# Optimization experiments

Measured on AMD Instinct MI355X. Metric: run time of the kernel, lower is better.

The kernel has to match this reference:

```python
import jax, jax.numpy as jnp
import numpy as np

N_CLASSES = 1000
FEAT_DIM = 256
N = 65536


def setup_inputs() -> dict:
    key = jax.random.key(0)
    k1, k2, k3 = jax.random.split(key, 3)
    gt = jax.random.randint(k1, (N, N_CLASSES), 0, 2, dtype=jnp.int32)
    features = jax.random.normal(k2, (N, FEAT_DIM), dtype=jnp.float32)
    centers = jax.random.normal(k3, (N_CLASSES, FEAT_DIM), dtype=jnp.float32)
    return {"gt": gt, "features": features, "centers": centers}


def reference(gt, features, centers):
    # loss = (1/N) * sum_c sum_{i : gt[i,c] > 0} ||features[i] - centers[c]||^2
    # Vectorized via ||f||^2 + ||c||^2 - 2 f.c  (replaces the per-class python loop)
    mask = (gt > 0).astype(features.dtype)                      # [N, C]
    f_sq = jnp.sum(features * features, axis=1)                 # [N]
    c_sq = jnp.sum(centers * centers, axis=1)                   # [C]
    cross = features @ centers.T                                # [N, C]
    dist = f_sq[:, None] + c_sq[None, :] - 2.0 * cross          # [N, C]
    num_instances = features.shape[0]
    return jnp.sum(mask * dist) / num_instances
```

## Files before the change

kernel.cpp:

```cpp
#include <hip/hip_runtime.h>
#include <stdint.h>

#define N_ROWS 65536
#define N_CLS  1000
#define KPAD   1024
#define FEAT   256
#define MT     64
#define BK     64
#define NIT    (KPAD/BK)

typedef _Float16 f16x8 __attribute__((ext_vector_type(8)));
typedef _Float16 f16x2 __attribute__((ext_vector_type(2)));
typedef float    f32x4 __attribute__((ext_vector_type(4)));

__device__ __forceinline__ f16x2 as_f16x2(uint32_t u) {
    union { uint32_t u; f16x2 h; } c; c.u = u; return c.h;
}

__global__ __launch_bounds__(256) void prep_kernel(const float* __restrict__ centers,
                                                   ushort* __restrict__ centersT,
                                                   ushort* __restrict__ csqh,
                                                   float* __restrict__ out) {
    const int c = blockIdx.x;
    const int n = threadIdx.x;
    float v = 0.f;
    if (c < N_CLS) v = centers[(size_t)c * FEAT + n];
    union { _Float16 h; ushort s; } cv; cv.h = (_Float16)v;
    centersT[(size_t)n * KPAD + c] = cv.s;
    float sq = v * v;
    #pragma unroll
    for (int off = 32; off > 0; off >>= 1) sq += __shfl_down(sq, off);
    __shared__ float red[4];
    if ((threadIdx.x & 63) == 0) red[threadIdx.x >> 6] = sq;
    __syncthreads();
    if (threadIdx.x == 0) {
        union { _Float16 h; ushort s; } cs;
        cs.h = (_Float16)(red[0] + red[1] + red[2] + red[3]);
        csqh[c] = cs.s;
        if (c == 0) out[0] = 0.f;
    }
}

__global__ __launch_bounds__(256, 4) void main_kernel(const int* __restrict__ gt,
                                                      const float* __restrict__ features,
                                                      const ushort* __restrict__ centersT,
                                                      const ushort* __restrict__ csqh,
                                                      float* __restrict__ out) {
    __shared__ uint4 As4[MT * 8];
    __shared__ uint4 Bs4[FEAT * 8];

    const int tid  = threadIdx.x;
    const int m0   = blockIdx.x * MT;
    const int r    = tid >> 2;
    const int kc2  = tid & 3;
    const int lane = tid & 63;
    const int w    = tid >> 6;
    const int ml   = lane & 15;
    const int quad = lane >> 4;
    const int mls  = ml & 7;

    f32x4 acc[4][4];
    #pragma unroll
    for (int i = 0; i < 4; i++)
        #pragma unroll
        for (int j = 0; j < 4; j++)
            #pragma unroll
            for (int k = 0; k < 4; k++) acc[i][j][k] = 0.f;

    uint32_t rcp = 0;
    float    t2  = 0.f;
    const int*   gtrow = gt + (size_t)(m0 + r) * N_CLS;
    const uint4* ctv   = (const uint4*)centersT;

    for (int it = 0; it < NIT; ++it) {
        const int k0 = it * BK;
        const int kb = k0 + kc2 * 16;
        __syncthreads();

        int v[16];
        if (kb + 16 <= N_CLS) {
            const int4* p = (const int4*)(gtrow + kb);
            int4 a0 = p[0], a1 = p[1], a2 = p[2], a3 = p[3];
            v[0]=a0.x; v[1]=a0.y; v[2]=a0.z; v[3]=a0.w;
            v[4]=a1.x; v[5]=a1.y; v[6]=a1.z; v[7]=a1.w;
            v[8]=a2.x; v[9]=a2.y; v[10]=a2.z; v[11]=a2.w;
            v[12]=a3.x; v[13]=a3.y; v[14]=a3.z; v[15]=a3.w;
        } else {
            #pragma unroll
            for (int j = 0; j < 16; j++) {
                int k = kb + j;
                v[j] = (k < N_CLS) ? gtrow[k] : 0;
            }
        }
        uint4 cq0 = *(const uint4*)(csqh + kb);
        uint4 cq1 = *(const uint4*)(csqh + kb + 8);
        uint32_t cp[8] = {cq0.x, cq0.y, cq0.z, cq0.w, cq1.x, cq1.y, cq1.z, cq1.w};

        uint32_t u[8];
        #pragma unroll
        for (int j = 0; j < 8; j++) {
            uint32_t t = (uint32_t)v[2*j] + ((uint32_t)v[2*j+1] << 16);
            rcp += t;
            u[j] = t * 0x3C00u;
            t2 = __builtin_amdgcn_fdot2(as_f16x2(u[j]), as_f16x2(cp[j]), t2, false);
        }

        {
            uint4* dst = &As4[r * 8];
            dst[(2*kc2)     ^ (r & 7)] = make_uint4(u[0], u[1], u[2], u[3]);
            dst[(2*kc2 + 1) ^ (r & 7)] = make_uint4(u[4], u[5], u[6], u[7]);
        }

        #pragma unroll
        for (int j = 0; j < 8; j++) {
            int g  = j * 256 + tid;
            int n  = g >> 3;
            int kl = g & 7;
            Bs4[n * 8 + (kl ^ (n & 7))] = ctv[n * 128 + (k0 >> 3) + kl];
        }

        __syncthreads();

        #pragma unroll
        for (int ks = 0; ks < 2; ++ks) {
            const int lc = ks * 4 + quad;
            f16x8 af[4], bfr[4];
            #pragma unroll
            for (int mt = 0; mt < 4; mt++)
                af[mt] = ((const f16x8*)As4)[(mt * 16 + ml) * 8 + (lc ^ mls)];
            #pragma unroll
            for (int nt = 0; nt < 4; nt++) {
                const int col = w * 64 + nt * 16 + ml;
                bfr[nt] = ((const f16x8*)Bs4)[col * 8 + (lc ^ mls)];
            }
            #pragma unroll
            for (int mt = 0; mt < 4; mt++)
                #pragma unroll
                for (int nt = 0; nt < 4; nt++)
                    acc[mt][nt] = __builtin_amdgcn_mfma_f32_16x16x32_f16(
                        af[mt], bfr[nt], acc[mt][nt], 0, 0, 0);
        }
    }

    __syncthreads();
    float* S = (float*)As4;
    S[tid] = (float)((rcp & 0xFFFFu) + (rcp >> 16));
    __syncthreads();
    if (tid < MT)
        S[256 + tid] = S[tid*4] + S[tid*4+1] + S[tid*4+2] + S[tid*4+3];
    __syncthreads();

    float part = t2;
    #pragma unroll
    for (int mt = 0; mt < 4; mt++) {
        #pragma unroll
        for (int nt = 0; nt < 4; nt++) {
            const int n = w * 64 + nt * 16 + ml;
            #pragma unroll
            for (int reg = 0; reg < 4; reg++) {
                const int ri = mt * 16 + quad * 4 + reg;
                const float f = features[(size_t)(m0 + ri) * FEAT + n];
                const float T = acc[mt][nt][reg];
                part += f * (S[256 + ri] * f - 2.f * T);
            }
        }
    }
    #pragma unroll
    for (int off = 32; off > 0; off >>= 1) part += __shfl_down(part, off);
    if (lane == 0) S[320 + w] = part;
    __syncthreads();
    if (tid == 0)
        atomicAdd(out, (S[320] + S[321] + S[322] + S[323]) * (1.f / (float)N_ROWS));
}

extern "C" void kernel_launch(void* const* d_in, const int* in_sizes, int n_in,
                              void* d_out, int out_size, void* d_ws, size_t ws_size,
                              hipStream_t stream) {
    const int*   gt       = (const int*)d_in[0];
    const float* features = (const float*)d_in[1];
    const float* centers  = (const float*)d_in[2];
    float*       out      = (float*)d_out;

    ushort* centersT = (ushort*)d_ws;
    ushort* csqh     = (ushort*)((char*)d_ws + (size_t)FEAT * KPAD * 2);

    prep_kernel<<<KPAD, 256, 0, stream>>>(centers, centersT, csqh, out);
    main_kernel<<<N_ROWS / MT, 256, 0, stream>>>(gt, features, centersT, csqh, out);
}
```

Before: 434.3 us.

## Give each wave its own 16-row tile and stream centers from global into registers

Each wave now handles its own 16 rows across all 256 features. The centers operand is loaded straight from global or L2 into registers with double buffering, instead of being staged through shared memory behind block-wide barriers. The next gt tile is prefetched into registers while the current MFMAs run, and the row-count reduction is done with wave shuffles. This removes the per-iteration __syncthreads and the shared-memory B staging. In exchange it uses more registers (occupancy hint lowered to 2) and does redundant global reads of centers per wave.

```diff
diff --git a/kernel.cpp b/kernel.cpp
--- a/kernel.cpp
+++ b/kernel.cpp
@@ -41,136 +41,149 @@
     }
 }
 
-__global__ __launch_bounds__(256, 4) void main_kernel(const int* __restrict__ gt,
+__global__ __launch_bounds__(256, 2) void main_kernel(const int* __restrict__ gt,
                                                       const float* __restrict__ features,
                                                       const ushort* __restrict__ centersT,
                                                       const ushort* __restrict__ csqh,
                                                       float* __restrict__ out) {
-    __shared__ uint4 As4[MT * 8];
-    __shared__ uint4 Bs4[FEAT * 8];
+    __shared__ uint4 As4[4][16 * 8];
+    __shared__ float red[4];
 
     const int tid  = threadIdx.x;
-    const int m0   = blockIdx.x * MT;
-    const int r    = tid >> 2;
-    const int kc2  = tid & 3;
     const int lane = tid & 63;
     const int w    = tid >> 6;
+    const int r    = lane >> 2;
+    const int kc   = lane & 3;
     const int ml   = lane & 15;
     const int quad = lane >> 4;
     const int mls  = ml & 7;
-
-    f32x4 acc[4][4];
-    #pragma unroll
-    for (int i = 0; i < 4; i++)
-        #pragma unroll
-        for (int j = 0; j < 4; j++)
-            #pragma unroll
-            for (int k = 0; k < 4; k++) acc[i][j][k] = 0.f;
+    const int mw   = blockIdx.x * MT + w * 16;
+
+    const int*    gtrow = gt + (size_t)(mw + r) * N_CLS;
+    const ushort* cb    = centersT + (size_t)ml * KPAD + quad * 8;
+    uint4*        AsW   = As4[w];
+
+    f32x4 acc[16];
+    #pragma unroll
+    for (int i = 0; i < 16; i++)
+        #pragma unroll
+        for (int k = 0; k < 4; k++) acc[i][k] = 0.f;
 
     uint32_t rcp = 0;
     float    t2  = 0.f;
-    const int*   gtrow = gt + (size_t)(m0 + r) * N_CLS;
-    const uint4* ctv   = (const uint4*)centersT;
+
+    int4 a0, a1, a2, a3;
+    {
+        const int4* p = (const int4*)(gtrow + kc * 16);
+        a0 = p[0]; a1 = p[1]; a2 = p[2]; a3 = p[3];
+    }
+
+    f16x8 b0[8], b1[8];
+    #pragma unroll
+    for (int nt = 0; nt < 8; nt++)
+        b0[nt] = *(const f16x8*)(cb + (size_t)(nt * 16) * KPAD);
 
     for (int it = 0; it < NIT; ++it) {
         const int k0 = it * BK;
-        const int kb = k0 + kc2 * 16;
-        __syncthreads();
-
-        int v[16];
-        if (kb + 16 <= N_CLS) {
-            const int4* p = (const int4*)(gtrow + kb);
-            int4 a0 = p[0], a1 = p[1], a2 = p[2], a3 = p[3];
-            v[0]=a0.x; v[1]=a0.y; v[2]=a0.z; v[3]=a0.w;
-            v[4]=a1.x; v[5]=a1.y; v[6]=a1.z; v[7]=a1.w;
-            v[8]=a2.x; v[9]=a2.y; v[10]=a2.z; v[11]=a2.w;
-            v[12]=a3.x; v[13]=a3.y; v[14]=a3.z; v[15]=a3.w;
-        } else {
-            #pragma unroll
-            for (int j = 0; j < 16; j++) {
-                int k = kb + j;
-                v[j] = (k < N_CLS) ? gtrow[k] : 0;
-            }
-        }
+
+        #pragma unroll
+        for (int nt = 0; nt < 8; nt++)
+            b1[nt] = *(const f16x8*)(cb + (size_t)((nt + 8) * 16) * KPAD + k0);
+
+        const int kb = k0 + kc * 16;
         uint4 cq0 = *(const uint4*)(csqh + kb);
         uint4 cq1 = *(const uint4*)(csqh + kb + 8);
-        uint32_t cp[8] = {cq0.x, cq0.y, cq0.z, cq0.w, cq1.x, cq1.y, cq1.z, cq1.w};
-
+        uint32_t cs[8] = {cq0.x, cq0.y, cq0.z, cq0.w, cq1.x, cq1.y, cq1.z, cq1.w};
+
+        int v[16] = {a0.x, a0.y, a0.z, a0.w, a1.x, a1.y, a1.z, a1.w,
+                     a2.x, a2.y, a2.z, a2.w, a3.x, a3.y, a3.z, a3.w};
         uint32_t u[8];
         #pragma unroll
         for (int j = 0; j < 8; j++) {
             uint32_t t = (uint32_t)v[2*j] + ((uint32_t)v[2*j+1] << 16);
             rcp += t;
             u[j] = t * 0x3C00u;
-            t2 = __builtin_amdgcn_fdot2(as_f16x2(u[j]), as_f16x2(cp[j]), t2, false);
-        }
-
-        {
-            uint4* dst = &As4[r * 8];
-            dst[(2*kc2)     ^ (r & 7)] = make_uint4(u[0], u[1], u[2], u[3]);
-            dst[(2*kc2 + 1) ^ (r & 7)] = make_uint4(u[4], u[5], u[6], u[7]);
-        }
-
-        #pragma unroll
-        for (int j = 0; j < 8; j++) {
-            int g  = j * 256 + tid;
-            int n  = g >> 3;
-            int kl = g & 7;
-            Bs4[n * 8 + (kl ^ (n & 7))] = ctv[n * 128 + (k0 >> 3) + kl];
-        }
-
-        __syncthreads();
-
-        #pragma unroll
-        for (int ks = 0; ks < 2; ++ks) {
-            const int lc = ks * 4 + quad;
-            f16x8 af[4], bfr[4];
+            t2 = __builtin_amdgcn_fdot2(as_f16x2(u[j]), as_f16x2(cs[j]), t2, false);
+        }
+
+        AsW[r * 8 + ((2*kc)     ^ (r & 7))] = make_uint4(u[0], u[1], u[2], u[3]);
+        AsW[r * 8 + ((2*kc + 1) ^ (r & 7))] = make_uint4(u[4], u[5], u[6], u[7]);
+
+        if (it + 1 < NIT) {
+            const int kb2 = (it + 1) * BK + kc * 16;
+            if (kb2 + 16 <= N_CLS) {
+                const int4* p = (const int4*)(gtrow + kb2);
+                a0 = p[0]; a1 = p[1]; a2 = p[2]; a3 = p[3];
+            } else {
+                int t16[16];
+                #pragma unroll
+                for (int j = 0; j < 16; j++) {
+                    int k = kb2 + j;
+                    t16[j] = (k < N_CLS) ? gtrow[k] : 0;
+                }
+                a0 = make_int4(t16[0],  t16[1],  t16[2],  t16[3]);
+                a1 = make_int4(t16[4],  t16[5],  t16[6],  t16[7]);
+                a2 = make_int4(t16[8],  t16[9],  t16[10], t16[11]);
+                a3 = make_int4(t16[12], t16[13], t16[14], t16[15]);
+            }
+        }
+
+        f16x8 af0 = ((const f16x8*)AsW)[ml * 8 + ( quad      ^ mls)];
+        f16x8 af1 = ((const f16x8*)AsW)[ml * 8 + ((4 + quad) ^ mls)];
+
+        #pragma unroll
+        for (int nt = 0; nt < 8; nt++)
+            acc[nt] = __builtin_amdgcn_mfma_f32_16x16x32_f16(af0, b0[nt], acc[nt], 0, 0, 0);
+        #pragma unroll
+        for (int nt = 0; nt < 8; nt++)
+            b0[nt] = *(const f16x8*)(cb + (size_t)(nt * 16) * KPAD + k0 + 32);
+
+        #pragma unroll
+        for (int nt = 0; nt < 8; nt++)
+            acc[8+nt] = __builtin_amdgcn_mfma_f32_16x16x32_f16(af0, b1[nt], acc[8+nt], 0, 0, 0);
+        #pragma unroll
+        for (int nt = 0; nt < 8; nt++)
+            b1[nt] = *(const f16x8*)(cb + (size_t)((nt + 8) * 16) * KPAD + k0 + 32);
+
+        #pragma unroll
+        for (int nt = 0; nt < 8; nt++)
+            acc[nt] = __builtin_amdgcn_mfma_f32_16x16x32_f16(af1, b0[nt], acc[nt], 0, 0, 0);
+        if (it + 1 < NIT) {
             #pragma unroll
-            for (int mt = 0; mt < 4; mt++)
-                af[mt] = ((const f16x8*)As4)[(mt * 16 + ml) * 8 + (lc ^ mls)];
-            #pragma unroll
-            for (int nt = 0; nt < 4; nt++) {
-                const int col = w * 64 + nt * 16 + ml;
-                bfr[nt] = ((const f16x8*)Bs4)[col * 8 + (lc ^ mls)];
-            }
-            #pragma unroll
-            for (int mt = 0; mt < 4; mt++)
-                #pragma unroll
-                for (int nt = 0; nt < 4; nt++)
-                    acc[mt][nt] = __builtin_amdgcn_mfma_f32_16x16x32_f16(
-                        af[mt], bfr[nt], acc[mt][nt], 0, 0, 0);
-        }
-    }
-
-    __syncthreads();
-    float* S = (float*)As4;
-    S[tid] = (float)((rcp & 0xFFFFu) + (rcp >> 16));
-    __syncthreads();
-    if (tid < MT)
-        S[256 + tid] = S[tid*4] + S[tid*4+1] + S[tid*4+2] + S[tid*4+3];
-    __syncthreads();
+            for (int nt = 0; nt < 8; nt++)
+                b0[nt] = *(const f16x8*)(cb + (size_t)(nt * 16) * KPAD + k0 + 64);
+        }
+
+        #pragma unroll
+        for (int nt = 0; nt < 8; nt++)
+            acc[8+nt] = __builtin_amdgcn_mfma_f32_16x16x32_f16(af1, b1[nt], acc[8+nt], 0, 0, 0);
+    }
+
+    float rcf = (float)((rcp & 0xFFFFu) + (rcp >> 16));
+    rcf += __shfl_xor(rcf, 1);
+    rcf += __shfl_xor(rcf, 2);
+    float rw[4];
+    #pragma unroll
+    for (int reg = 0; reg < 4; reg++)
+        rw[reg] = __shfl(rcf, quad * 16 + reg * 4);
 
     float part = t2;
     #pragma unroll
-    for (int mt = 0; mt < 4; mt++) {
-        #pragma unroll
-        for (int nt = 0; nt < 4; nt++) {
-            const int n = w * 64 + nt * 16 + ml;
-            #pragma unroll
-            for (int reg = 0; reg < 4; reg++) {
-                const int ri = mt * 16 + quad * 4 + reg;
-                const float f = features[(size_t)(m0 + ri) * FEAT + n];
-                const float T = acc[mt][nt][reg];
-                part += f * (S[256 + ri] * f - 2.f * T);
-            }
+    for (int nt = 0; nt < 16; nt++) {
+        const int n = nt * 16 + ml;
+        #pragma unroll
+        for (int reg = 0; reg < 4; reg++) {
+            const int ri = quad * 4 + reg;
+            const float f = features[(size_t)(mw + ri) * FEAT + n];
+            part += f * (rw[reg] * f - 2.f * acc[nt][reg]);
         }
     }
     #pragma unroll
     for (int off = 32; off > 0; off >>= 1) part += __shfl_down(part, off);
-    if (lane == 0) S[320 + w] = part;
+    if (lane == 0) red[w] = part;
     __syncthreads();
     if (tid == 0)
-        atomicAdd(out, (S[320] + S[321] + S[322] + S[323]) * (1.f / (float)N_ROWS));
+        atomicAdd(out, (red[0] + red[1] + red[2] + red[3]) * (1.f / (float)N_ROWS));
 }
 
 extern "C" void kernel_launch(void* const* d_in, const int* in_sizes, int n_in,
```

Measured after the change: 582.3 us. 1.34x slower.

## Preload gt tile into LDS bitmask panel with flat coalesced loads

Applied to the files above, without the earlier changes.

Before the GEMM loop, the whole 64x1000 gt tile for the block is read with flat, fully contiguous int4 loads. Each group of 8 entries is compressed into one byte of an LDS bitmask panel, and the c_sq dot term is accumulated in fp32 at the same time. The MFMA loop then rebuilds the fp16 A fragments from those bits, and row counts come from popcounts over the panel. This removes the per-row strided gt loads and the fp16 A tile staging inside the main loop. The cost is a separate load phase that does not overlap with compute, plus bit-expansion ALU work in the inner loop.

```diff
diff --git a/kernel.cpp b/kernel.cpp
--- a/kernel.cpp
+++ b/kernel.cpp
@@ -6,20 +6,26 @@
 #define KPAD   1024
 #define FEAT   256
 #define MT     64
-#define BK     64
-#define NIT    (KPAD/BK)
+#define NIT    16
+#define PITERS 16
 
 typedef _Float16 f16x8 __attribute__((ext_vector_type(8)));
-typedef _Float16 f16x2 __attribute__((ext_vector_type(2)));
 typedef float    f32x4 __attribute__((ext_vector_type(4)));
 
-__device__ __forceinline__ f16x2 as_f16x2(uint32_t u) {
-    union { uint32_t u; f16x2 h; } c; c.u = u; return c.h;
+__device__ __forceinline__ f16x8 expand8(uint32_t b) {
+    union { uint32_t u[4]; f16x8 v; } r;
+#pragma unroll
+    for (int p = 0; p < 4; ++p) {
+        uint32_t lo = (b >> (2 * p)) & 1u;
+        uint32_t hi = (b >> (2 * p + 1)) & 1u;
+        r.u[p] = lo * 0x3C00u + hi * 0x3C000000u;
+    }
+    return r.v;
 }
 
 __global__ __launch_bounds__(256) void prep_kernel(const float* __restrict__ centers,
                                                    ushort* __restrict__ centersT,
-                                                   ushort* __restrict__ csqh,
+                                                   float* __restrict__ csqf,
                                                    float* __restrict__ out) {
     const int c = blockIdx.x;
     const int n = threadIdx.x;
@@ -28,15 +34,13 @@
     union { _Float16 h; ushort s; } cv; cv.h = (_Float16)v;
     centersT[(size_t)n * KPAD + c] = cv.s;
     float sq = v * v;
-    #pragma unroll
+#pragma unroll
     for (int off = 32; off > 0; off >>= 1) sq += __shfl_down(sq, off);
     __shared__ float red[4];
     if ((threadIdx.x & 63) == 0) red[threadIdx.x >> 6] = sq;
     __syncthreads();
     if (threadIdx.x == 0) {
-        union { _Float16 h; ushort s; } cs;
-        cs.h = (_Float16)(red[0] + red[1] + red[2] + red[3]);
-        csqh[c] = cs.s;
+        csqf[c] = red[0] + red[1] + red[2] + red[3];
         if (c == 0) out[0] = 0.f;
     }
 }
@@ -44,133 +48,139 @@
 __global__ __launch_bounds__(256, 4) void main_kernel(const int* __restrict__ gt,
                                                       const float* __restrict__ features,
                                                       const ushort* __restrict__ centersT,
-                                                      const ushort* __restrict__ csqh,
+                                                      const float* __restrict__ csqf,
                                                       float* __restrict__ out) {
-    __shared__ uint4 As4[MT * 8];
     __shared__ uint4 Bs4[FEAT * 8];
+    __shared__ uint4 panelV[512];
+    unsigned char* panel = (unsigned char*)panelV;
 
     const int tid  = threadIdx.x;
     const int m0   = blockIdx.x * MT;
-    const int r    = tid >> 2;
-    const int kc2  = tid & 3;
     const int lane = tid & 63;
     const int w    = tid >> 6;
     const int ml   = lane & 15;
     const int quad = lane >> 4;
     const int mls  = ml & 7;
 
+    panelV[tid]       = make_uint4(0, 0, 0, 0);
+    panelV[256 + tid] = make_uint4(0, 0, 0, 0);
+
     f32x4 acc[4][4];
-    #pragma unroll
+#pragma unroll
     for (int i = 0; i < 4; i++)
-        #pragma unroll
+#pragma unroll
         for (int j = 0; j < 4; j++)
-            #pragma unroll
+#pragma unroll
             for (int k = 0; k < 4; k++) acc[i][j][k] = 0.f;
 
-    uint32_t rcp = 0;
-    float    t2  = 0.f;
-    const int*   gtrow = gt + (size_t)(m0 + r) * N_CLS;
-    const uint4* ctv   = (const uint4*)centersT;
+    float t2 = 0.f;
+    const int* gtb = gt + (size_t)m0 * N_CLS;
 
-    for (int it = 0; it < NIT; ++it) {
-        const int k0 = it * BK;
-        const int kb = k0 + kc2 * 16;
-        __syncthreads();
+    __syncthreads();
 
-        int v[16];
-        if (kb + 16 <= N_CLS) {
-            const int4* p = (const int4*)(gtrow + kb);
-            int4 a0 = p[0], a1 = p[1], a2 = p[2], a3 = p[3];
-            v[0]=a0.x; v[1]=a0.y; v[2]=a0.z; v[3]=a0.w;
-            v[4]=a1.x; v[5]=a1.y; v[6]=a1.z; v[7]=a1.w;
-            v[8]=a2.x; v[9]=a2.y; v[10]=a2.z; v[11]=a2.w;
-            v[12]=a3.x; v[13]=a3.y; v[14]=a3.z; v[15]=a3.w;
-        } else {
-            #pragma unroll
-            for (int j = 0; j < 16; j++) {
-                int k = kb + j;
-                v[j] = (k < N_CLS) ? gtrow[k] : 0;
+#pragma unroll 1
+    for (int p = 0; p < PITERS; ++p) {
+        const int o = p * 4096 + tid * 16;
+        if (o < MT * N_CLS) {
+            const int4* src = (const int4*)(gtb + o);
+            int4 q0 = src[0], q1 = src[1], q2 = src[2], q3 = src[3];
+            const int vv[16] = {q0.x, q0.y, q0.z, q0.w, q1.x, q1.y, q1.z, q1.w,
+                                q2.x, q2.y, q2.z, q2.w, q3.x, q3.y, q3.z, q3.w};
+#pragma unroll
+            for (int h = 0; h < 2; ++h) {
+                const uint32_t ob = (uint32_t)(o + h * 8);
+                const uint32_t r = (ob * 67109u) >> 26;
+                const uint32_t c = ob - r * 1000u;
+                const float4* cp = (const float4*)(csqf + c);
+                float4 s0 = cp[0], s1 = cp[1];
+                const float cs[8] = {s0.x, s0.y, s0.z, s0.w, s1.x, s1.y, s1.z, s1.w};
+                uint32_t m = 0;
+#pragma unroll
+                for (int j = 0; j < 8; ++j) {
+                    const bool bit = vv[h * 8 + j] > 0;
+                    m |= (uint32_t)bit << j;
+                    t2 += bit ? cs[j] : 0.f;
+                }
+                panel[r * 128 + (c >> 3)] = (unsigned char)m;
             }
         }
-        uint4 cq0 = *(const uint4*)(csqh + kb);
-        uint4 cq1 = *(const uint4*)(csqh + kb + 8);
-        uint32_t cp[8] = {cq0.x, cq0.y, cq0.z, cq0.w, cq1.x, cq1.y, cq1.z, cq1.w};
+    }
 
-        uint32_t u[8];
-        #pragma unroll
-        for (int j = 0; j < 8; j++) {
-            uint32_t t = (uint32_t)v[2*j] + ((uint32_t)v[2*j+1] << 16);
-            rcp += t;
-            u[j] = t * 0x3C00u;
-            t2 = __builtin_amdgcn_fdot2(as_f16x2(u[j]), as_f16x2(cp[j]), t2, false);
+    __syncthreads();
+
+    const uint4* ctv = (const uint4*)centersT;
+    for (int it = 0; it < NIT; ++it) {
+        if (it) __syncthreads();
+#pragma unroll
+        for (int j = 0; j < 8; ++j) {
+            const int g = j * 256 + tid;
+            const int n = g >> 3;
+            const int kl = g & 7;
+            Bs4[n * 8 + (kl ^ (n & 7))] = ctv[n * 128 + it * 8 + kl];
         }
-
-        {
-            uint4* dst = &As4[r * 8];
-            dst[(2*kc2)     ^ (r & 7)] = make_uint4(u[0], u[1], u[2], u[3]);
-            dst[(2*kc2 + 1) ^ (r & 7)] = make_uint4(u[4], u[5], u[6], u[7]);
-        }
-
-        #pragma unroll
-        for (int j = 0; j < 8; j++) {
-            int g  = j * 256 + tid;
-            int n  = g >> 3;
-            int kl = g & 7;
-            Bs4[n * 8 + (kl ^ (n & 7))] = ctv[n * 128 + (k0 >> 3) + kl];
-        }
-
+        uint2 bits[4];
+#pragma unroll
+        for (int mt = 0; mt < 4; ++mt)
+            bits[mt] = *(const uint2*)(panel + (mt * 16 + ml) * 128 + it * 8);
         __syncthreads();
-
-        #pragma unroll
+#pragma unroll
         for (int ks = 0; ks < 2; ++ks) {
+            f16x8 af[4], bfr[4];
+#pragma unroll
+            for (int mt = 0; mt < 4; ++mt) {
+                const uint32_t by = ((ks ? bits[mt].y : bits[mt].x) >> (8 * quad)) & 0xFFu;
+                af[mt] = expand8(by);
+            }
             const int lc = ks * 4 + quad;
-            f16x8 af[4], bfr[4];
-            #pragma unroll
-            for (int mt = 0; mt < 4; mt++)
-                af[mt] = ((const f16x8*)As4)[(mt * 16 + ml) * 8 + (lc ^ mls)];
-            #pragma unroll
-            for (int nt = 0; nt < 4; nt++) {
-                const int col = w * 64 + nt * 16 + ml;
-                bfr[nt] = ((const f16x8*)Bs4)[col * 8 + (lc ^ mls)];
-            }
-            #pragma unroll
-            for (int mt = 0; mt < 4; mt++)
-                #pragma unroll
-                for (int nt = 0; nt < 4; nt++)
+#pragma unroll
+            for (int nt = 0; nt < 4; ++nt)
+                bfr[nt] = ((const f16x8*)Bs4)[(w * 64 + nt * 16 + ml) * 8 + (lc ^ mls)];
+#pragma unroll
+            for (int mt = 0; mt < 4; ++mt)
+#pragma unroll
+                for (int nt = 0; nt < 4; ++nt)
                     acc[mt][nt] = __builtin_amdgcn_mfma_f32_16x16x32_f16(
                         af[mt], bfr[nt], acc[mt][nt], 0, 0, 0);
         }
     }
 
     __syncthreads();
-    float* S = (float*)As4;
-    S[tid] = (float)((rcp & 0xFFFFu) + (rcp >> 16));
-    __syncthreads();
-    if (tid < MT)
-        S[256 + tid] = S[tid*4] + S[tid*4+1] + S[tid*4+2] + S[tid*4+3];
+
+    {
+        const int row = tid >> 2, part = tid & 3;
+        const uint4* rp = (const uint4*)(panel + row * 128 + part * 32);
+        uint4 x = rp[0], y = rp[1];
+        float cnt = (float)(__popc(x.x) + __popc(x.y) + __popc(x.z) + __popc(x.w) +
+                            __popc(y.x) + __popc(y.y) + __popc(y.z) + __popc(y.w));
+        cnt += __shfl_xor(cnt, 1);
+        cnt += __shfl_xor(cnt, 2);
+        if (part == 0) ((float*)Bs4)[row] = cnt;
+    }
     __syncthreads();
 
-    float part = t2;
-    #pragma unroll
-    for (int mt = 0; mt < 4; mt++) {
-        #pragma unroll
-        for (int nt = 0; nt < 4; nt++) {
+    const float* rowcntL = (const float*)Bs4;
+    float ps = t2;
+#pragma unroll
+    for (int mt = 0; mt < 4; ++mt) {
+#pragma unroll
+        for (int nt = 0; nt < 4; ++nt) {
             const int n = w * 64 + nt * 16 + ml;
-            #pragma unroll
-            for (int reg = 0; reg < 4; reg++) {
+#pragma unroll
+            for (int reg = 0; reg < 4; ++reg) {
                 const int ri = mt * 16 + quad * 4 + reg;
                 const float f = features[(size_t)(m0 + ri) * FEAT + n];
-                const float T = acc[mt][nt][reg];
-                part += f * (S[256 + ri] * f - 2.f * T);
+                ps += f * (rowcntL[ri] * f - 2.f * acc[mt][nt][reg]);
             }
         }
     }
-    #pragma unroll
-    for (int off = 32; off > 0; off >>= 1) part += __shfl_down(part, off);
-    if (lane == 0) S[320 + w] = part;
+#pragma unroll
+    for (int off = 32; off > 0; off >>= 1) ps += __shfl_down(ps, off);
+    if (lane == 0) ((float*)Bs4)[64 + w] = ps;
     __syncthreads();
-    if (tid == 0)
-        atomicAdd(out, (S[320] + S[321] + S[322] + S[323]) * (1.f / (float)N_ROWS));
+    if (tid == 0) {
+        const float* S = (const float*)Bs4;
+        atomicAdd(out, (S[64] + S[65] + S[66] + S[67]) * (1.f / (float)N_ROWS));
+    }
 }
 
 extern "C" void kernel_launch(void* const* d_in, const int* in_sizes, int n_in,
@@ -182,8 +192,8 @@
     float*       out      = (float*)d_out;
 
     ushort* centersT = (ushort*)d_ws;
-    ushort* csqh     = (ushort*)((char*)d_ws + (size_t)FEAT * KPAD * 2);
+    float*  csqf     = (float*)((char*)d_ws + (size_t)FEAT * KPAD * 2);
 
-    prep_kernel<<<KPAD, 256, 0, stream>>>(centers, centersT, csqh, out);
-    main_kernel<<<N_ROWS / MT, 256, 0, stream>>>(gt, features, centersT, csqh, out);
+    prep_kernel<<<KPAD, 256, 0, stream>>>(centers, centersT, csqf, out);
+    main_kernel<<<N_ROWS / MT, 256, 0, stream>>>(gt, features, centersT, csqf, out);
 }
```

After: 446.5 us. 2.8% more time.
